# Performance work log

Measured on AMD Instinct MI355X. Metric: run time of the kernel, lower is better.

The kernel has to match this reference:

```python
import jax, jax.numpy as jnp
import numpy as np

EPS = 1e-06

def _splat_dists(t, centers):
    # t: [B,T,H,Dh], centers: [H,S,Dh] -> euclidean dists [B,T,H,S] (torch.cdist)
    t_sq = jnp.sum(t * t, axis=-1, keepdims=True)          # [B,T,H,1]
    c_sq = jnp.sum(centers * centers, axis=-1)             # [H,S]
    dots = jnp.einsum('bthd,hsd->bths', t, centers)        # [B,T,H,S]
    d2 = jnp.maximum(t_sq + c_sq[None, None] - 2.0 * dots, 0.0)
    return jnp.sqrt(d2)


def setup_inputs() -> dict:
    key = jax.random.key(0)
    ks = jax.random.split(key, 6)
    B, T, D, H, S = 2, 2048, 1024, 8, 32
    Dh = D // H
    scale = 1.0 / np.sqrt(D)
    return {
        'x': jax.random.normal(ks[0], (B, T, D), jnp.float32),
        'Wqkv': jax.random.normal(ks[1], (D, 3 * D), jnp.float32) * scale,
        'bqkv': jnp.zeros((3 * D,), jnp.float32),
        'Wout': jax.random.normal(ks[2], (D, D), jnp.float32) * scale,
        'bout': jnp.zeros((D,), jnp.float32),
        'splat_centers': jax.random.normal(ks[3], (H, S, Dh), jnp.float32) * 0.5,
        'splat_log_scales': jnp.zeros((H, S), jnp.float32),
        'splat_log_amplitudes': jnp.zeros((H, S), jnp.float32),
        'temperature': jnp.ones((1,), jnp.float32),
    }


def reference(x, Wqkv, bqkv, Wout, bout, splat_centers, splat_log_scales,
              splat_log_amplitudes, temperature):
    B, T, D = x.shape
    H, S, Dh = splat_centers.shape
    qkv = (x @ Wqkv + bqkv).reshape(B, T, 3, H, Dh)
    q, k, v = qkv[:, :, 0], qkv[:, :, 1], qkv[:, :, 2]     # [B,T,H,Dh]

    q_dists = _splat_dists(q, splat_centers)               # [B,T,H,S]
    k_dists = _splat_dists(k, splat_centers)               # [B,T,H,S]

    scales = jnp.exp(splat_log_scales)[None, None]         # [1,1,H,S]
    q_weights = jnp.exp(-0.5 * (q_dists / (scales + EPS)) ** 2)
    k_weights = jnp.exp(-0.5 * (k_dists / (scales + EPS)) ** 2)

    amplitudes = jnp.exp(splat_log_amplitudes)             # [H,S]
    # bihs,bjhs,hs -> bijh : fold amplitudes into q_weights first
    qa = q_weights * amplitudes[None, None]
    logits = jnp.einsum('bihs,bjhs->bijh', qa, k_weights) / temperature[0]
    attention = jax.nn.softmax(logits, axis=2)             # softmax over j
    out = jnp.einsum('bijh,bjhd->bihd', attention, v).reshape(B, T, D)
    return out @ Wout + bout, attention
```

## Files before the change

### kernel.cpp

```cpp
#include <hip/hip_runtime.h>
#include <math.h>


typedef __attribute__((ext_vector_type(8))) short s16x8;
typedef __attribute__((ext_vector_type(4))) short s16x4;
typedef __attribute__((ext_vector_type(4))) float f32x4;

__device__ inline short f2bf(float f) {
  union { float f; unsigned u; } v; v.f = f;
  unsigned r = v.u + 0x7FFFu + ((v.u >> 16) & 1u);
  return (short)(r >> 16);
}
__device__ inline unsigned cvt_pk_bf16(float lo, float hi) {
  unsigned r;
  asm("v_cvt_pk_bf16_f32 %0, %1, %2" : "=v"(r) : "v"(lo), "v"(hi));
  return r;
}
#define MFMA_BF16(a, b, c) __builtin_amdgcn_mfma_f32_16x16x32_bf16((a), (b), (c), 0, 0, 0)

#define GLOAD_LDS16(gsrc, ldst)                                          \
  __builtin_amdgcn_global_load_lds(                                      \
      (const __attribute__((address_space(1))) void*)(gsrc),             \
      (__attribute__((address_space(3))) void*)(ldst), 16, 0, 0)

__device__ inline void transpose_tile32(const float* __restrict__ W,
                                        short* __restrict__ Wt, int K, int N,
                                        int n0, int k0) {
  __shared__ float tile[32][33];
  const int r = threadIdx.x >> 3, c4 = (threadIdx.x & 7) * 4;
  float4 v = *(const float4*)(W + (size_t)(k0 + r) * N + n0 + c4);
  tile[r][c4 + 0] = v.x; tile[r][c4 + 1] = v.y;
  tile[r][c4 + 2] = v.z; tile[r][c4 + 3] = v.w;
  __syncthreads();
  s16x4 o;
  o[0] = f2bf(tile[c4 + 0][r]);
  o[1] = f2bf(tile[c4 + 1][r]);
  o[2] = f2bf(tile[c4 + 2][r]);
  o[3] = f2bf(tile[c4 + 3][r]);
  *(s16x4*)(Wt + (size_t)(n0 + r) * K + k0 + c4) = o;
}

__global__ __launch_bounds__(256) void prep_fused(
    const float* __restrict__ x, short* __restrict__ x16,
    const float* __restrict__ Wqkv, short* __restrict__ Wqt16,
    const float* __restrict__ Wout, short* __restrict__ Wot16,
    const float* __restrict__ ctr, const float* __restrict__ ls,
    const float* __restrict__ la, short* __restrict__ c16,
    float* __restrict__ csq, float* __restrict__ inv2, float* __restrict__ amp) {
  const int bx = blockIdx.x;
  if (bx < 4096) {
    int i = bx * 256 + threadIdx.x;
    float4 v = ((const float4*)x)[i];
    s16x4 o;
    o[0] = f2bf(v.x); o[1] = f2bf(v.y); o[2] = f2bf(v.z); o[3] = f2bf(v.w);
    ((s16x4*)x16)[i] = o;
  } else if (bx < 7168) {
    int idx = bx - 4096;
    transpose_tile32(Wqkv, Wqt16, 1024, 3072, (idx % 96) * 32, (idx / 96) * 32);
  } else if (bx < 8192) {
    int idx = bx - 7168;
    transpose_tile32(Wout, Wot16, 1024, 1024, (idx % 32) * 32, (idx / 32) * 32);
  } else {
    const int t = threadIdx.x;
    float sumsq = 0.f;
#pragma unroll
    for (int d = 0; d < 128; d += 4) {
      float4 v = *(const float4*)(ctr + (size_t)t * 128 + d);
      sumsq += v.x * v.x + v.y * v.y + v.z * v.z + v.w * v.w;
      s16x4 o;
      o[0] = f2bf(v.x); o[1] = f2bf(v.y); o[2] = f2bf(v.z); o[3] = f2bf(v.w);
      *(s16x4*)(c16 + (size_t)t * 128 + d) = o;
    }
    csq[t] = sumsq;
    float sc = __expf(ls[t]);
    float iv = 1.0f / (sc + 1e-6f);
    inv2[t] = -0.5f * iv * iv;
    amp[t] = __expf(la[t]);
  }
}

template <int N, bool SCATTER>
__global__ __launch_bounds__(256) void gemm_bf16(
    const short* __restrict__ A, const short* __restrict__ Wt,
    const float* __restrict__ bias,
    float* __restrict__ out0, float* __restrict__ out1, float* __restrict__ out2) {
  __shared__ short As[128 * 64];
  __shared__ short Bs[128 * 64];
  const int tid = threadIdx.x;
  const int w = tid >> 6, l = tid & 63;
  const int lm = l & 15, lk = l >> 4;
  const int bn0 = blockIdx.x * 128;
  const int bm0 = blockIdx.y * 128;
  const int n0 = bn0 + (w & 1) * 64;
  const int m0 = bm0 + (w >> 1) * 64;
  const int K = 1024;
  f32x4 acc[4][4];
#pragma unroll
  for (int mi = 0; mi < 4; mi++)
#pragma unroll
    for (int ni = 0; ni < 4; ni++) acc[mi][ni] = (f32x4){0.f, 0.f, 0.f, 0.f};

  const int srow = l >> 3;
  const int scol = (l & 7) * 8;
  const int mh = (w >> 1) * 64, nh = (w & 1) * 64;

  for (int k0 = 0; k0 < K; k0 += 64) {
#pragma unroll
    for (int q = 0; q < 4; q++) {
      const int chunk = w * 4 + q;
      const int row = chunk * 8 + srow;
      GLOAD_LDS16(A + (size_t)(bm0 + row) * K + k0 + scol, As + chunk * 512);
      GLOAD_LDS16(Wt + (size_t)(bn0 + row) * K + k0 + scol, Bs + chunk * 512);
    }
    __syncthreads();
#pragma unroll
    for (int kk = 0; kk < 2; kk++) {
      s16x8 af[4], bf[4];
#pragma unroll
      for (int i = 0; i < 4; i++) {
        af[i] = *(const s16x8*)(As + (mh + i * 16 + lm) * 64 + kk * 32 + lk * 8);
        bf[i] = *(const s16x8*)(Bs + (nh + i * 16 + lm) * 64 + kk * 32 + lk * 8);
      }
#pragma unroll
      for (int mi = 0; mi < 4; mi++)
#pragma unroll
        for (int ni = 0; ni < 4; ni++)
          acc[mi][ni] = MFMA_BF16(af[mi], bf[ni], acc[mi][ni]);
    }
    __syncthreads();
  }
#pragma unroll
  for (int ni = 0; ni < 4; ni++) {
    const int n = n0 + ni * 16 + lm;
    const float bv = bias[n];
#pragma unroll
    for (int mi = 0; mi < 4; mi++) {
#pragma unroll
      for (int r = 0; r < 4; r++) {
        const int m = m0 + mi * 16 + lk * 4 + r;
        float v = acc[mi][ni][r] + bv;
        if (SCATTER) {
          int three = n >> 10;
          int h = (n >> 7) & 7;
          int dh = n & 127;
          int bb = m >> 11, tt = m & 2047;
          float* dst = (three == 0) ? out0 : ((three == 1) ? out1 : out2);
          dst[((size_t)(bb * 8 + h) * 2048 + tt) * 128 + dh] = v;
        } else {
          out0[(size_t)m * N + n] = v;
        }
      }
    }
  }
}

__global__ __launch_bounds__(256) void splat_tv(
    const float* __restrict__ qT, const float* __restrict__ kT,
    const short* __restrict__ c16, const float* __restrict__ csq,
    const float* __restrict__ inv2, const float* __restrict__ amp,
    short* __restrict__ qa16, short* __restrict__ kw16,
    const float* __restrict__ vT, short* __restrict__ vt16) {
  __shared__ float tile[32][33];
  const int tid = threadIdx.x;
  if (blockIdx.x < 1024) {
    const int it = blockIdx.x & 31;
    const int bh = (blockIdx.x >> 5) & 15;
    const int which = blockIdx.x >> 9;
    const int w = tid >> 6, l = tid & 63;
    const int lm = l & 15, lk = l >> 4;
    const int h = bh & 7;
    const int i0 = it * 64 + w * 16;
    const float* src = which ? kT : qT;

    s16x8 af[4];
    float sq = 0.f;
#pragma unroll
    for (int kk = 0; kk < 4; kk++) {
      const float* p = src + ((size_t)bh * 2048 + i0 + lm) * 128 + kk * 32 + lk * 8;
      float4 v0 = *(const float4*)p;
      float4 v1 = *(const float4*)(p + 4);
      sq += v0.x * v0.x + v0.y * v0.y + v0.z * v0.z + v0.w * v0.w +
            v1.x * v1.x + v1.y * v1.y + v1.z * v1.z + v1.w * v1.w;
      af[kk][0] = f2bf(v0.x); af[kk][1] = f2bf(v0.y);
      af[kk][2] = f2bf(v0.z); af[kk][3] = f2bf(v0.w);
      af[kk][4] = f2bf(v1.x); af[kk][5] = f2bf(v1.y);
      af[kk][6] = f2bf(v1.z); af[kk][7] = f2bf(v1.w);
    }
    sq += __shfl_xor(sq, 16);
    sq += __shfl_xor(sq, 32);

    f32x4 acc[2];
    acc[0] = (f32x4){0.f, 0.f, 0.f, 0.f};
    acc[1] = (f32x4){0.f, 0.f, 0.f, 0.f};
#pragma unroll
    for (int kk = 0; kk < 4; kk++) {
      s16x8 b0 = *(const s16x8*)(c16 + (size_t)(h * 32 + lm) * 128 + kk * 32 + lk * 8);
      s16x8 b1 = *(const s16x8*)(c16 + (size_t)(h * 32 + 16 + lm) * 128 + kk * 32 + lk * 8);
      acc[0] = MFMA_BF16(af[kk], b0, acc[0]);
      acc[1] = MFMA_BF16(af[kk], b1, acc[1]);
    }
    short* dst = which ? kw16 : qa16;
#pragma unroll
    for (int ni = 0; ni < 2; ni++) {
      const int n = ni * 16 + lm;
      const float cs = csq[h * 32 + n];
      const float iv2 = inv2[h * 32 + n];
      const float am = which ? 1.0f : amp[h * 32 + n];
#pragma unroll
      for (int r = 0; r < 4; r++) {
        float qs = __shfl(sq, lk * 4 + r);
        float d2 = fmaxf(qs + cs - 2.0f * acc[ni][r], 0.0f);
        float wv = __expf(iv2 * d2) * am;
        int m = i0 + lk * 4 + r;
        dst[((size_t)bh * 2048 + m) * 32 + n] = f2bf(wv);
      }
    }
  } else {
    const int idx = blockIdx.x - 1024;
    const int t0 = (idx & 63) * 32;
    const int d0 = ((idx >> 6) & 3) * 32;
    const int bh = idx >> 8;
    const int r = tid >> 3, c4 = (tid & 7) * 4;
    float4 v = *(const float4*)(vT + ((size_t)(bh * 2048 + t0 + r)) * 128 + d0 + c4);
    tile[r][c4 + 0] = v.x; tile[r][c4 + 1] = v.y;
    tile[r][c4 + 2] = v.z; tile[r][c4 + 3] = v.w;
    __syncthreads();
    s16x4 o;
    o[0] = f2bf(tile[c4 + 0][r]);
    o[1] = f2bf(tile[c4 + 1][r]);
    o[2] = f2bf(tile[c4 + 2][r]);
    o[3] = f2bf(tile[c4 + 3][r]);
    *(s16x4*)(vt16 + ((size_t)(bh * 128 + d0 + r)) * 2048 + t0 + c4) = o;
  }
}

__global__ __launch_bounds__(256) void attn_flash(
    const short* __restrict__ qa16, const short* __restrict__ kw16,
    const short* __restrict__ vt16, const float* __restrict__ temp,
    float* __restrict__ lrow, short* __restrict__ aout16) {
  __shared__ short Vs[2][8192];
  const int tid = threadIdx.x;
  const int w = tid >> 6, l = tid & 63;
  const int lm = l & 15, lk = l >> 4;
  const int it = blockIdx.x, h = blockIdx.y;
  const int b = blockIdx.z;
  const int bh = b * 8 + h;
  const int i0 = it * 64 + w * 16;
  const float invT = 1.0f / temp[0];
  const short* kwb = kw16 + (size_t)bh * 2048 * 32;
  const short* vtb = vt16 + (size_t)bh * 128 * 2048;
  s16x8 qfrag = *(const s16x8*)(qa16 + ((size_t)(bh * 2048 + i0 + lm)) * 32 + lk * 8);
  float lsum = 0.f;
  f32x4 acc[8];
#pragma unroll
  for (int d = 0; d < 8; d++) acc[d] = (f32x4){0.f, 0.f, 0.f, 0.f};

  const int sig0 = (lm >> 2) * 8 + (lm & 3);
  const int srow8 = l >> 3;
  const int scb = (l & 7) ^ srow8;
  const int rcb0 = (lk ^ (lm & 7)) * 8;
  const int rcb1 = ((lk + 4) ^ (lm & 7)) * 8;

#pragma unroll
  for (int q = 0; q < 4; q++) {
    const int chunk = w * 4 + q;
    GLOAD_LDS16(vtb + (size_t)(chunk * 8 + srow8) * 2048 + scb * 8,
                &Vs[0][chunk * 512]);
  }
  __syncthreads();

  int cur = 0;
  for (int jc = 0; jc < 2048; jc += 64) {
    if (jc + 64 < 2048) {
#pragma unroll
      for (int q = 0; q < 4; q++) {
        const int chunk = w * 4 + q;
        GLOAD_LDS16(vtb + (size_t)(chunk * 8 + srow8) * 2048 + (jc + 64) + scb * 8,
                    &Vs[cur ^ 1][chunk * 512]);
      }
    }
    s16x8 kb[4];
    kb[0] = *(const s16x8*)(kwb + (size_t)(jc + sig0) * 32 + lk * 8);
    kb[1] = *(const s16x8*)(kwb + (size_t)(jc + sig0 + 4) * 32 + lk * 8);
    kb[2] = *(const s16x8*)(kwb + (size_t)(jc + sig0 + 32) * 32 + lk * 8);
    kb[3] = *(const s16x8*)(kwb + (size_t)(jc + sig0 + 36) * 32 + lk * 8);
    f32x4 z = (f32x4){0.f, 0.f, 0.f, 0.f};
    f32x4 s[4];
#pragma unroll
    for (int c = 0; c < 4; c++) s[c] = MFMA_BF16(kb[c], qfrag, z);
    float p[4][4];
#pragma unroll
    for (int c = 0; c < 4; c++) {
      p[c][0] = __expf(s[c][0] * invT);
      p[c][1] = __expf(s[c][1] * invT);
      p[c][2] = __expf(s[c][2] * invT);
      p[c][3] = __expf(s[c][3] * invT);
      lsum += (p[c][0] + p[c][1]) + (p[c][2] + p[c][3]);
    }
    union { unsigned u[4]; s16x8 v; } t0, t1;
    t0.u[0] = cvt_pk_bf16(p[0][0], p[0][1]);
    t0.u[1] = cvt_pk_bf16(p[0][2], p[0][3]);
    t0.u[2] = cvt_pk_bf16(p[1][0], p[1][1]);
    t0.u[3] = cvt_pk_bf16(p[1][2], p[1][3]);
    t1.u[0] = cvt_pk_bf16(p[2][0], p[2][1]);
    t1.u[1] = cvt_pk_bf16(p[2][2], p[2][3]);
    t1.u[2] = cvt_pk_bf16(p[3][0], p[3][1]);
    t1.u[3] = cvt_pk_bf16(p[3][2], p[3][3]);
    s16x8 pf0 = t0.v, pf1 = t1.v;
    const short* vb = Vs[cur];
#pragma unroll
    for (int d = 0; d < 8; d++) {
      const short* vsrow = vb + (d * 16 + lm) * 64;
      s16x8 vb0 = *(const s16x8*)(vsrow + rcb0);
      s16x8 vb1 = *(const s16x8*)(vsrow + rcb1);
      acc[d] = MFMA_BF16(pf0, vb0, acc[d]);
      acc[d] = MFMA_BF16(pf1, vb1, acc[d]);
    }
    __syncthreads();
    cur ^= 1;
  }
  lsum += __shfl_xor(lsum, 16);
  lsum += __shfl_xor(lsum, 32);
  if (l < 16) lrow[bh * 2048 + i0 + l] = lsum;
  float invl[4];
#pragma unroll
  for (int r = 0; r < 4; r++) invl[r] = 1.0f / __shfl(lsum, lk * 4 + r);
  short* ob = aout16 + ((size_t)(b * 2048 + i0)) * 1024 + h * 128 + lm;
#pragma unroll
  for (int r = 0; r < 4; r++) {
    const int row = lk * 4 + r;
#pragma unroll
    for (int d = 0; d < 8; d++)
      ob[(size_t)row * 1024 + d * 16] = f2bf(acc[d][r] * invl[r]);
  }
}

__global__ __launch_bounds__(256) void gemm_out(
    const short* __restrict__ aout16, const short* __restrict__ Wot16,
    const float* __restrict__ bout, float* __restrict__ out) {
  __shared__ short As[128 * 64];
  __shared__ short Bs[128 * 64];
  const int tid = threadIdx.x;
  const int w = tid >> 6, l = tid & 63;
  const int lm = l & 15, lk = l >> 4;
  const int idx = blockIdx.x;
  const int bn0 = (idx & 7) * 128;
  const int bm0 = (idx >> 3) * 128;
  const int n0 = bn0 + (w & 1) * 64;
  const int m0 = bm0 + (w >> 1) * 64;
  const int K = 1024;
  f32x4 acc[4][4];
#pragma unroll
  for (int mi = 0; mi < 4; mi++)
#pragma unroll
    for (int ni = 0; ni < 4; ni++) acc[mi][ni] = (f32x4){0.f, 0.f, 0.f, 0.f};
  const int srow = l >> 3;
  const int scol = (l & 7) * 8;
  const int mh = (w >> 1) * 64, nh = (w & 1) * 64;
  for (int k0 = 0; k0 < K; k0 += 64) {
#pragma unroll
    for (int q = 0; q < 4; q++) {
      const int chunk = w * 4 + q;
      const int row = chunk * 8 + srow;
      GLOAD_LDS16(aout16 + (size_t)(bm0 + row) * K + k0 + scol, As + chunk * 512);
      GLOAD_LDS16(Wot16 + (size_t)(bn0 + row) * K + k0 + scol, Bs + chunk * 512);
    }
    __syncthreads();
#pragma unroll
    for (int kk = 0; kk < 2; kk++) {
      s16x8 af[4], bf[4];
#pragma unroll
      for (int i = 0; i < 4; i++) {
        af[i] = *(const s16x8*)(As + (mh + i * 16 + lm) * 64 + kk * 32 + lk * 8);
        bf[i] = *(const s16x8*)(Bs + (nh + i * 16 + lm) * 64 + kk * 32 + lk * 8);
      }
#pragma unroll
      for (int mi = 0; mi < 4; mi++)
#pragma unroll
        for (int ni = 0; ni < 4; ni++)
          acc[mi][ni] = MFMA_BF16(af[mi], bf[ni], acc[mi][ni]);
    }
    __syncthreads();
  }
#pragma unroll
  for (int ni = 0; ni < 4; ni++) {
    const int n = n0 + ni * 16 + lm;
    const float bv = bout[n];
#pragma unroll
    for (int mi = 0; mi < 4; mi++) {
#pragma unroll
      for (int r = 0; r < 4; r++) {
        const int m = m0 + mi * 16 + lk * 4 + r;
        out[(size_t)m * 1024 + n] = acc[mi][ni][r] + bv;
      }
    }
  }
}

__global__ __launch_bounds__(256) void attn_write(
    const short* __restrict__ qa16, const short* __restrict__ kw16,
    const float* __restrict__ lrow, const float* __restrict__ temp,
    float* __restrict__ attn) {
  __shared__ float pl[8][16][33];
  const int tid = threadIdx.x;
  const int w = tid >> 6, l = tid & 63;
  const int lm = l & 15, lk = l >> 4;
  const int bx = blockIdx.x;
  const int i0 = (bx & 127) * 16;
  const int j0 = ((bx >> 7) & 63) * 32;
  const int b = bx >> 13;
  const float invT = 1.0f / temp[0];
#pragma unroll
  for (int hh = 0; hh < 2; hh++) {
    const int h = w * 2 + hh;
    const int bh = b * 8 + h;
    s16x8 qf = *(const s16x8*)(qa16 + ((size_t)(bh * 2048 + i0 + lm)) * 32 + lk * 8);
    s16x8 kf[2];
#pragma unroll
    for (int jh = 0; jh < 2; jh++)
      kf[jh] = *(const s16x8*)(kw16 + ((size_t)(bh * 2048 + j0 + jh * 16 + lm)) * 32 + lk * 8);
    float il[4];
#pragma unroll
    for (int r = 0; r < 4; r++)
      il[r] = 1.0f / lrow[bh * 2048 + i0 + lk * 4 + r];
    f32x4 z = (f32x4){0.f, 0.f, 0.f, 0.f};
#pragma unroll
    for (int jh = 0; jh < 2; jh++) {
      f32x4 s = MFMA_BF16(qf, kf[jh], z);
#pragma unroll
      for (int r = 0; r < 4; r++) {
        float p = __expf(s[r] * invT) * il[r];
        pl[h][lk * 4 + r][jh * 16 + lm] = p;
      }
    }
  }
  __syncthreads();
#pragma unroll
  for (int c = 0; c < 4; c++) {
    int u = c * 256 + tid;
    int i = u >> 6, rem = u & 63;
    int j = rem >> 1, h4 = (rem & 1) * 4;
    f32x4 v;
    v[0] = pl[h4][i][j];
    v[1] = pl[h4 + 1][i][j];
    v[2] = pl[h4 + 2][i][j];
    v[3] = pl[h4 + 3][i][j];
    f32x4* dst = (f32x4*)(attn + (((size_t)(b * 2048 + i0 + i)) * 2048 + j0 + j) * 8 + h4);
    __builtin_nontemporal_store(v, dst);
  }
}

extern "C" void kernel_launch(void* const* d_in, const int* in_sizes, int n_in,
                              void* d_out, int out_size, void* d_ws, size_t ws_size,
                              hipStream_t stream) {
  const float* x    = (const float*)d_in[0];
  const float* Wqkv = (const float*)d_in[1];
  const float* bqkv = (const float*)d_in[2];
  const float* Wout = (const float*)d_in[3];
  const float* bout = (const float*)d_in[4];
  const float* ctr  = (const float*)d_in[5];
  const float* ls   = (const float*)d_in[6];
  const float* la   = (const float*)d_in[7];
  const float* temp = (const float*)d_in[8];

  float* out = (float*)d_out;
  float* attn = out + 4194304;

  float* ws = (float*)d_ws;
  float* qT    = ws;
  float* kT    = qT + 4194304;
  float* vT    = kT + 4194304;
  short* x16   = (short*)(vT + 4194304);
  short* Wqt16 = x16 + 4194304;
  short* Wot16 = Wqt16 + 3145728;
  short* qa16  = Wot16 + 1048576;
  short* kw16  = qa16 + 1048576;
  float* lrow  = (float*)(kw16 + 1048576);
  float* csq   = lrow + 32768;
  float* inv2  = csq + 256;
  float* amp   = inv2 + 256;
  short* c16   = (short*)(amp + 256);
  short* vt16  = (short*)ws;
  short* aout16 = (short*)vT;

  prep_fused<<<8193, 256, 0, stream>>>(x, x16, Wqkv, Wqt16, Wout, Wot16,
                                       ctr, ls, la, c16, csq, inv2, amp);
  gemm_bf16<3072, true><<<dim3(24, 32), 256, 0, stream>>>(
      x16, Wqt16, bqkv, qT, kT, vT);
  splat_tv<<<5120, 256, 0, stream>>>(
      qT, kT, c16, csq, inv2, amp, qa16, kw16, vT, vt16);
  attn_flash<<<dim3(32, 8, 2), 256, 0, stream>>>(
      qa16, kw16, vt16, temp, lrow, aout16);
  gemm_out<<<256, 256, 0, stream>>>(aout16, Wot16, bout, out);
  attn_write<<<16384, 256, 0, stream>>>(qa16, kw16, lrow, temp, attn);
}
```

Measured before the change: 465.2 us.

## Emit bf16 q/k and transposed V directly from QKV GEMM epilogue

The QKV GEMM epilogue now converts outputs to bf16 and writes q and k in head-major layout and V already transposed, instead of fp32 intermediates. The splat kernel reads bf16 q/k and drops its V-transpose blocks, and the workspace layout is reorganized. This cuts intermediate memory traffic and one transpose pass. The cost is scattered 2-byte stores for the V transpose and norms computed from bf16-rounded values.

```diff
diff --git a/kernel.cpp b/kernel.cpp
--- a/kernel.cpp
+++ b/kernel.cpp
@@ -10,6 +10,11 @@
   union { float f; unsigned u; } v; v.f = f;
   unsigned r = v.u + 0x7FFFu + ((v.u >> 16) & 1u);
   return (short)(r >> 16);
+}
+__device__ inline float bf2f(short s) {
+  union { unsigned u; float f; } v;
+  v.u = ((unsigned)(unsigned short)s) << 16;
+  return v.f;
 }
 __device__ inline unsigned cvt_pk_bf16(float lo, float hi) {
   unsigned r;
@@ -83,7 +88,8 @@
 __global__ __launch_bounds__(256) void gemm_bf16(
     const short* __restrict__ A, const short* __restrict__ Wt,
     const float* __restrict__ bias,
-    float* __restrict__ out0, float* __restrict__ out1, float* __restrict__ out2) {
+    short* __restrict__ q16, short* __restrict__ k16, short* __restrict__ vt16,
+    float* __restrict__ outf) {
   __shared__ short As[128 * 64];
   __shared__ short Bs[128 * 64];
   const int tid = threadIdx.x;
@@ -144,10 +150,15 @@
           int h = (n >> 7) & 7;
           int dh = n & 127;
           int bb = m >> 11, tt = m & 2047;
-          float* dst = (three == 0) ? out0 : ((three == 1) ? out1 : out2);
-          dst[((size_t)(bb * 8 + h) * 2048 + tt) * 128 + dh] = v;
+          int bh = bb * 8 + h;
+          if (three == 0)
+            q16[((size_t)bh * 2048 + tt) * 128 + dh] = f2bf(v);
+          else if (three == 1)
+            k16[((size_t)bh * 2048 + tt) * 128 + dh] = f2bf(v);
+          else
+            vt16[((size_t)(bh * 128 + dh)) * 2048 + tt] = f2bf(v);
         } else {
-          out0[(size_t)m * N + n] = v;
+          outf[(size_t)m * N + n] = v;
         }
       }
     }
@@ -155,82 +166,59 @@
 }
 
 __global__ __launch_bounds__(256) void splat_tv(
-    const float* __restrict__ qT, const float* __restrict__ kT,
+    const short* __restrict__ q16, const short* __restrict__ k16,
     const short* __restrict__ c16, const float* __restrict__ csq,
     const float* __restrict__ inv2, const float* __restrict__ amp,
-    short* __restrict__ qa16, short* __restrict__ kw16,
-    const float* __restrict__ vT, short* __restrict__ vt16) {
-  __shared__ float tile[32][33];
+    short* __restrict__ qa16, short* __restrict__ kw16) {
   const int tid = threadIdx.x;
-  if (blockIdx.x < 1024) {
-    const int it = blockIdx.x & 31;
-    const int bh = (blockIdx.x >> 5) & 15;
-    const int which = blockIdx.x >> 9;
-    const int w = tid >> 6, l = tid & 63;
-    const int lm = l & 15, lk = l >> 4;
-    const int h = bh & 7;
-    const int i0 = it * 64 + w * 16;
-    const float* src = which ? kT : qT;
-
-    s16x8 af[4];
-    float sq = 0.f;
-#pragma unroll
-    for (int kk = 0; kk < 4; kk++) {
-      const float* p = src + ((size_t)bh * 2048 + i0 + lm) * 128 + kk * 32 + lk * 8;
-      float4 v0 = *(const float4*)p;
-      float4 v1 = *(const float4*)(p + 4);
-      sq += v0.x * v0.x + v0.y * v0.y + v0.z * v0.z + v0.w * v0.w +
-            v1.x * v1.x + v1.y * v1.y + v1.z * v1.z + v1.w * v1.w;
-      af[kk][0] = f2bf(v0.x); af[kk][1] = f2bf(v0.y);
-      af[kk][2] = f2bf(v0.z); af[kk][3] = f2bf(v0.w);
-      af[kk][4] = f2bf(v1.x); af[kk][5] = f2bf(v1.y);
-      af[kk][6] = f2bf(v1.z); af[kk][7] = f2bf(v1.w);
-    }
-    sq += __shfl_xor(sq, 16);
-    sq += __shfl_xor(sq, 32);
-
-    f32x4 acc[2];
-    acc[0] = (f32x4){0.f, 0.f, 0.f, 0.f};
-    acc[1] = (f32x4){0.f, 0.f, 0.f, 0.f};
-#pragma unroll
-    for (int kk = 0; kk < 4; kk++) {
-      s16x8 b0 = *(const s16x8*)(c16 + (size_t)(h * 32 + lm) * 128 + kk * 32 + lk * 8);
-      s16x8 b1 = *(const s16x8*)(c16 + (size_t)(h * 32 + 16 + lm) * 128 + kk * 32 + lk * 8);
-      acc[0] = MFMA_BF16(af[kk], b0, acc[0]);
-      acc[1] = MFMA_BF16(af[kk], b1, acc[1]);
-    }
-    short* dst = which ? kw16 : qa16;
-#pragma unroll
-    for (int ni = 0; ni < 2; ni++) {
-      const int n = ni * 16 + lm;
-      const float cs = csq[h * 32 + n];
-      const float iv2 = inv2[h * 32 + n];
-      const float am = which ? 1.0f : amp[h * 32 + n];
-#pragma unroll
-      for (int r = 0; r < 4; r++) {
-        float qs = __shfl(sq, lk * 4 + r);
-        float d2 = fmaxf(qs + cs - 2.0f * acc[ni][r], 0.0f);
-        float wv = __expf(iv2 * d2) * am;
-        int m = i0 + lk * 4 + r;
-        dst[((size_t)bh * 2048 + m) * 32 + n] = f2bf(wv);
-      }
-    }
-  } else {
-    const int idx = blockIdx.x - 1024;
-    const int t0 = (idx & 63) * 32;
-    const int d0 = ((idx >> 6) & 3) * 32;
-    const int bh = idx >> 8;
-    const int r = tid >> 3, c4 = (tid & 7) * 4;
-    float4 v = *(const float4*)(vT + ((size_t)(bh * 2048 + t0 + r)) * 128 + d0 + c4);
-    tile[r][c4 + 0] = v.x; tile[r][c4 + 1] = v.y;
-    tile[r][c4 + 2] = v.z; tile[r][c4 + 3] = v.w;
-    __syncthreads();
-    s16x4 o;
-    o[0] = f2bf(tile[c4 + 0][r]);
-    o[1] = f2bf(tile[c4 + 1][r]);
-    o[2] = f2bf(tile[c4 + 2][r]);
-    o[3] = f2bf(tile[c4 + 3][r]);
-    *(s16x4*)(vt16 + ((size_t)(bh * 128 + d0 + r)) * 2048 + t0 + c4) = o;
+  const int it = blockIdx.x & 31;
+  const int bh = (blockIdx.x >> 5) & 15;
+  const int which = blockIdx.x >> 9;
+  const int w = tid >> 6, l = tid & 63;
+  const int lm = l & 15, lk = l >> 4;
+  const int h = bh & 7;
+  const int i0 = it * 64 + w * 16;
+  const short* src = which ? k16 : q16;
+
+  s16x8 af[4];
+  float sq = 0.f;
+#pragma unroll
+  for (int kk = 0; kk < 4; kk++) {
+    af[kk] = *(const s16x8*)(src + ((size_t)bh * 2048 + i0 + lm) * 128 + kk * 32 + lk * 8);
+#pragma unroll
+    for (int j = 0; j < 8; j++) {
+      float f = bf2f(af[kk][j]);
+      sq += f * f;
+    }
+  }
+  sq += __shfl_xor(sq, 16);
+  sq += __shfl_xor(sq, 32);
+
+  f32x4 acc[2];
+  acc[0] = (f32x4){0.f, 0.f, 0.f, 0.f};
+  acc[1] = (f32x4){0.f, 0.f, 0.f, 0.f};
+#pragma unroll
+  for (int kk = 0; kk < 4; kk++) {
+    s16x8 b0 = *(const s16x8*)(c16 + (size_t)(h * 32 + lm) * 128 + kk * 32 + lk * 8);
+    s16x8 b1 = *(const s16x8*)(c16 + (size_t)(h * 32 + 16 + lm) * 128 + kk * 32 + lk * 8);
+    acc[0] = MFMA_BF16(af[kk], b0, acc[0]);
+    acc[1] = MFMA_BF16(af[kk], b1, acc[1]);
+  }
+  short* dst = which ? kw16 : qa16;
+#pragma unroll
+  for (int ni = 0; ni < 2; ni++) {
+    const int n = ni * 16 + lm;
+    const float cs = csq[h * 32 + n];
+    const float iv2 = inv2[h * 32 + n];
+    const float am = which ? 1.0f : amp[h * 32 + n];
+#pragma unroll
+    for (int r = 0; r < 4; r++) {
+      float qs = __shfl(sq, lk * 4 + r);
+      float d2 = fmaxf(qs + cs - 2.0f * acc[ni][r], 0.0f);
+      float wv = __expf(iv2 * d2) * am;
+      int m = i0 + lk * 4 + r;
+      dst[((size_t)bh * 2048 + m) * 32 + n] = f2bf(wv);
+    }
   }
 }
 
@@ -466,29 +454,28 @@
   float* out = (float*)d_out;
   float* attn = out + 4194304;
 
-  float* ws = (float*)d_ws;
-  float* qT    = ws;
-  float* kT    = qT + 4194304;
-  float* vT    = kT + 4194304;
-  short* x16   = (short*)(vT + 4194304);
+  short* ws16 = (short*)d_ws;
+  short* q16   = ws16;
+  short* k16   = q16 + 4194304;
+  short* vt16  = k16 + 4194304;
+  short* x16   = vt16 + 4194304;
   short* Wqt16 = x16 + 4194304;
   short* Wot16 = Wqt16 + 3145728;
   short* qa16  = Wot16 + 1048576;
   short* kw16  = qa16 + 1048576;
-  float* lrow  = (float*)(kw16 + 1048576);
+  short* aout16 = kw16 + 1048576;
+  short* c16   = aout16 + 4194304;
+  float* lrow  = (float*)(c16 + 32768);
   float* csq   = lrow + 32768;
   float* inv2  = csq + 256;
   float* amp   = inv2 + 256;
-  short* c16   = (short*)(amp + 256);
-  short* vt16  = (short*)ws;
-  short* aout16 = (short*)vT;
 
   prep_fused<<<8193, 256, 0, stream>>>(x, x16, Wqkv, Wqt16, Wout, Wot16,
                                        ctr, ls, la, c16, csq, inv2, amp);
   gemm_bf16<3072, true><<<dim3(24, 32), 256, 0, stream>>>(
-      x16, Wqt16, bqkv, qT, kT, vT);
-  splat_tv<<<5120, 256, 0, stream>>>(
-      qT, kT, c16, csq, inv2, amp, qa16, kw16, vT, vt16);
+      x16, Wqt16, bqkv, q16, k16, vt16, nullptr);
+  splat_tv<<<1024, 256, 0, stream>>>(
+      q16, k16, c16, csq, inv2, amp, qa16, kw16);
   attn_flash<<<dim3(32, 8, 2), 256, 0, stream>>>(
       qa16, kw16, vt16, temp, lrow, aout16);
   gemm_out<<<256, 256, 0, stream>>>(aout16, Wot16, bout, out);
```

After: 472.9 us. Within noise of the previous version (+1.7%).
